# Optimization experiments

Hardware: AMD Instinct MI355X
Metric: run time of the kernel (lower is better)

Reference implementation:

```python
import jax, jax.numpy as jnp
import numpy as np

N_TOTAL = 100000   # total nodes across types
NP_TYPE = 50000    # nodes per type
NP_G = 50000       # nodes per metapath graph
E_G = 500000       # edges per metapath graph
NH = 4             # attention heads
HD = 64            # per-head hidden dim
HID = 64           # shared hidden dim (== in_dim)
D = NH * HD        # 256, semantic attention dim
OUT = 64
T = 20000          # target nodes per metapath


def setup_inputs() -> dict:
    key = jax.random.key(0)
    ks = jax.random.split(key, 20)
    inp = {
        "features0": jax.random.normal(ks[0], (NP_TYPE, 256), jnp.float32),
        "features1": jax.random.normal(ks[1], (NP_TYPE, 256), jnp.float32),
        "fc_W": jax.random.normal(ks[2], (2, HID, 256), jnp.float32) * 0.06,
        "fc_b": jnp.zeros((2, HID), jnp.float32),
        "gat_W": jax.random.normal(ks[3], (2, 2, HID, D), jnp.float32) * 0.12,
        "attn_l": jax.random.normal(ks[4], (2, 2, NH, HD), jnp.float32) * 0.12,
        "attn_r": jax.random.normal(ks[5], (2, 2, NH, HD), jnp.float32) * 0.12,
        "sem_W": jax.random.normal(ks[6], (2, D, D), jnp.float32) * 0.06,
        "sem_b": jnp.zeros((2, D), jnp.float32),
        "sem_q": jax.random.normal(ks[7], (2, D), jnp.float32) * 0.06,
        "fcout_W": jax.random.normal(ks[8], (2, D, OUT), jnp.float32) * 0.06,
        "fcout_b": jnp.zeros((2, OUT), jnp.float32),
        # static index structure (== np.where(type_mask == i))
        "type_idx": jnp.arange(2 * NP_TYPE, dtype=jnp.int32).reshape(2, NP_TYPE),
        "node_idx": jax.random.randint(ks[9], (2, 2, NP_G), 0, N_TOTAL, jnp.int32),
        "edge_src": jax.random.randint(ks[10], (2, 2, E_G), 0, NP_G, jnp.int32),
        "edge_dst": jax.random.randint(ks[11], (2, 2, E_G), 0, NP_G, jnp.int32),
        "tgt_idx": jax.random.randint(ks[12], (2, 2, T), 0, NP_G, jnp.int32),
    }
    return inp


def _gat(h, W, al, ar, src, dst):
    # h: [NP_G, HID] -> multi-head GAT -> [NP_G, NH*HD]
    z = (h @ W).reshape(NP_G, NH, HD)
    el = jnp.sum(z * al, axis=-1)                     # [NP_G, NH]
    er = jnp.sum(z * ar, axis=-1)
    e = jax.nn.leaky_relu(el[src] + er[dst], 0.2)     # [E, NH]
    emax = jax.ops.segment_max(e, dst, num_segments=NP_G)
    emax = jnp.where(jnp.isfinite(emax), emax, 0.0)
    ex = jnp.exp(e - emax[dst])
    denom = jax.ops.segment_sum(ex, dst, num_segments=NP_G)
    alpha = ex / (denom[dst] + 1e-9)                  # edge softmax over in-edges
    out = jax.ops.segment_sum(alpha[:, :, None] * z[src], dst, num_segments=NP_G)
    return jax.nn.elu(out).reshape(NP_G, D)


def _semantic(zs, Wm, bm, qm):
    # zs: [T, M, D] metapath-specific embeddings
    w = jnp.mean(jnp.tanh(zs @ Wm + bm) @ qm, axis=0)  # [M]
    beta = jax.nn.softmax(w)
    return jnp.einsum('tmd,m->td', zs, beta)


def reference(features0, features1, fc_W, fc_b, gat_W, attn_l, attn_r,
              sem_W, sem_b, sem_q, fcout_W, fcout_b,
              type_idx, node_idx, edge_src, edge_dst, tgt_idx):
    # type-based linear + scatter into shared node-feature tensor
    transformed = jnp.zeros((N_TOTAL, HID), dtype=features0.dtype)
    transformed = transformed.at[type_idx[0]].set(features0 @ fc_W[0].T + fc_b[0])
    transformed = transformed.at[type_idx[1]].set(features1 @ fc_W[1].T + fc_b[1])

    outs = []
    for b in range(2):          # two HAN branches (gene, dis)
        metas = []
        for m in range(2):      # metapaths per branch
            h = transformed[node_idx[b, m]]            # gather metapath node feats
            o = _gat(h, gat_W[b, m], attn_l[b, m], attn_r[b, m],
                     edge_src[b, m], edge_dst[b, m])
            metas.append(o[tgt_idx[b, m]])             # select target nodes
        zs = jnp.stack(metas, axis=1)                  # [T, M, D]
        s = _semantic(zs, sem_W[b], sem_b[b], sem_q[b])
        outs.append(s @ fcout_W[b] + fcout_b[b])
    return jnp.stack(outs)  # [2, T, OUT]
```

## Files before the change

### kernel.cpp

```cpp
#include <hip/hip_runtime.h>
#include <math.h>

#define NT     100000
#define NPT    50000
#define NPG    50000
#define EG     500000
#define DD     256
#define TT     20000
#define NPB    196

typedef __attribute__((ext_vector_type(8))) short short8;
typedef __attribute__((ext_vector_type(4))) float f32x4;
typedef unsigned short u16;

#define MFMA16(a, b, c) __builtin_amdgcn_mfma_f32_16x16x32_bf16((a), (b), (c), 0, 0, 0)

__device__ inline unsigned pk2(float x, float y) {
    unsigned a = __float_as_uint(x); a = (a + 0x7FFFu + ((a >> 16) & 1u)) >> 16;
    unsigned b = __float_as_uint(y); b = (b + 0x7FFFu + ((b >> 16) & 1u)) >> 16;
    return (a & 0xFFFFu) | (b << 16);
}
__device__ inline u16 pkb(float x) {
    unsigned a = __float_as_uint(x);
    return (u16)((a + 0x7FFFu + ((a >> 16) & 1u)) >> 16);
}
__device__ inline short8 cvt8(float4 a, float4 b) {
    union { int4 i; short8 s; } u;
    u.i = make_int4((int)pk2(a.x, a.y), (int)pk2(a.z, a.w),
                    (int)pk2(b.x, b.y), (int)pk2(b.z, b.w));
    return u.s;
}
__device__ inline float4 up4(unsigned lo, unsigned hi) {
    float4 r;
    r.x = __uint_as_float(lo << 16);
    r.y = __uint_as_float(lo & 0xFFFF0000u);
    r.z = __uint_as_float(hi << 16);
    r.w = __uint_as_float(hi & 0xFFFF0000u);
    return r;
}
__device__ inline float uplo(unsigned w) { return __uint_as_float(w << 16); }
__device__ inline float uphi(unsigned w) { return __uint_as_float(w & 0xFFFF0000u); }
__device__ inline float ftanh(float x) {
    float e = __expf(2.f * x);
    return 1.f - 2.f * __builtin_amdgcn_rcpf(e + 1.f);
}

__global__ __launch_bounds__(256) void prep_kernel(
    const float* __restrict__ fcW, const float* __restrict__ gatW,
    const float* __restrict__ semW, const float* __restrict__ foW,
    u16* __restrict__ fcWb, u16* __restrict__ gatWb,
    u16* __restrict__ semWb, u16* __restrict__ foWb)
{
    int i = blockIdx.x * 256 + threadIdx.x;
    if (i < 32768) fcWb[i] = pkb(fcW[i]);
    if (i < 65536) {
        int g = i >> 14, rem = i & 16383, n = rem >> 6, k = rem & 63;
        gatWb[i] = pkb(gatW[g * 16384 + k * 256 + n]);
    }
    if (i < 131072) {
        int b = i >> 16, rem = i & 65535, n = rem >> 8, k = rem & 255;
        semWb[i] = pkb(semW[b * 65536 + k * 256 + n]);
    }
    if (i < 32768) {
        int b = i >> 14, rem = i & 16383, n = rem >> 8, k = rem & 255;
        foWb[i] = pkb(foW[b * 16384 + k * 64 + n]);
    }
}

__global__ __launch_bounds__(256) void fc_kernel(
    const float* __restrict__ f0, const float* __restrict__ f1,
    const u16* __restrict__ fcWb, const float* __restrict__ fcb,
    const int* __restrict__ type_idx, u16* __restrict__ tbf)
{
    __shared__ short As[64 * 256];
    __shared__ short Bs[64 * 256];
    int ty = blockIdx.y;
    const float* feat = ty ? f1 : f0;
    const u16* W = fcWb + ty * 64 * 256;
    int tid = threadIdx.x, wv = tid >> 6, l = tid & 63, q = l >> 4, c = l & 15;
    int rbase = blockIdx.x * 64;
    short8 bv[8];
#pragma unroll
    for (int j = 0; j < 8; ++j)
        bv[j] = *(const short8*)&W[(tid + 256 * j) * 8];
    const float* Abase = feat + (size_t)rbase * 256;
#pragma unroll
    for (int half = 0; half < 2; ++half) {
        float4 va[8];
#pragma unroll
        for (int j = 0; j < 8; ++j) {
            int fi = tid + 256 * (half * 8 + j);
            bool okA = (rbase + (fi >> 6)) < NPT;
            va[j] = okA ? *(const float4*)(Abase + (size_t)fi * 4)
                        : (float4){0.f, 0.f, 0.f, 0.f};
        }
#pragma unroll
        for (int j = 0; j < 8; ++j) {
            int fi = tid + 256 * (half * 8 + j);
            int r = fi >> 6, cs = (fi & 63) * 4;
            int2 v = make_int2((int)pk2(va[j].x, va[j].y),
                               (int)pk2(va[j].z, va[j].w));
            *(int2*)&As[r * 256 + (cs ^ ((r & 15) << 3))] = v;
        }
    }
#pragma unroll
    for (int j = 0; j < 8; ++j) {
        int e = tid + 256 * j, r = e >> 5, cs = (e & 31) * 8;
        *(short8*)&Bs[r * 256 + (cs ^ ((r & 15) << 3))] = bv[j];
    }
    __syncthreads();
    short8 af[8];
    int arow = wv * 16 + c;
#pragma unroll
    for (int s = 0; s < 8; ++s)
        af[s] = *(const short8*)&As[arow * 256 + ((q * 8 + 32 * s) ^ (c << 3))];
    f32x4 acc[4];
#pragma unroll
    for (int i = 0; i < 4; ++i) acc[i] = (f32x4){0.f, 0.f, 0.f, 0.f};
#pragma unroll
    for (int s = 0; s < 8; ++s)
#pragma unroll
        for (int t4 = 0; t4 < 4; ++t4)
            acc[t4] = MFMA16(af[s],
                *(const short8*)&Bs[(t4 * 16 + c) * 256 +
                                    ((q * 8 + 32 * s) ^ (c << 3))], acc[t4]);
    int grl = rbase + wv * 16 + q * 4;
#pragma unroll
    for (int t4 = 0; t4 < 4; ++t4) {
        int col = t4 * 16 + c;
        float bvv = fcb[ty * 64 + col];
#pragma unroll
        for (int reg = 0; reg < 4; ++reg) {
            int gr = grl + reg;
            if (gr < NPT) {
                int dest = type_idx[ty * NPT + gr];
                tbf[(size_t)dest * 64 + col] = pkb(acc[t4][reg] + bvv);
            }
        }
    }
}

__global__ __launch_bounds__(256) void z_kernel(
    const u16* __restrict__ tbf, const int* __restrict__ nidx4,
    const u16* __restrict__ gatWb4, const float* __restrict__ al4,
    const float* __restrict__ ar4, u16* __restrict__ zb4,
    float* __restrict__ el4, float* __restrict__ er4, int g0)
{
    __shared__ short Bs[256 * 72];
    int gy = blockIdx.y, g = g0 + gy;
    const int* nidx = nidx4 + (size_t)g * NPG;
    const u16* gatWb = gatWb4 + (size_t)g * 16384;
    const float* al = al4 + g * 256;
    const float* ar = ar4 + g * 256;
    u16* zb = zb4 + (size_t)gy * NPG * 256;
    float* el = el4 + (size_t)gy * NPG * 4;
    float* er = er4 + (size_t)gy * NPG * 4;
    int tid = threadIdx.x, wv = tid >> 6, l = tid & 63, q = l >> 4, c = l & 15;
    short8 bv[8];
#pragma unroll
    for (int j = 0; j < 8; ++j)
        bv[j] = *(const short8*)&gatWb[(tid + 256 * j) * 8];
    int rbase = blockIdx.x * 64;
    int row = rbase + wv * 16 + c;
    bool ok = row < NPG;
    short8 af0 = (short8)(short)0, af1 = (short8)(short)0;
    if (ok) {
        int n = nidx[row];
        const u16* Ap = tbf + (size_t)n * 64 + q * 8;
        af0 = *(const short8*)(Ap);
        af1 = *(const short8*)(Ap + 32);
    }
#pragma unroll
    for (int j = 0; j < 8; ++j) {
        int e = tid + 256 * j, r = e >> 3, kc = (e & 7) * 8;
        *(short8*)&Bs[r * 72 + kc] = bv[j];
    }
    __syncthreads();
    f32x4 acc[16];
    const f32x4 zero = (f32x4){0.f, 0.f, 0.f, 0.f};
#pragma unroll
    for (int t16 = 0; t16 < 16; ++t16) {
        const short* Bp = &Bs[(t16 * 16 + c) * 72 + q * 8];
        acc[t16] = MFMA16(af0, *(const short8*)&Bp[0], zero);
        acc[t16] = MFMA16(af1, *(const short8*)&Bp[32], acc[t16]);
    }
    int grl = rbase + wv * 16 + q * 4;
#pragma unroll
    for (int t16 = 0; t16 < 16; ++t16)
#pragma unroll
        for (int reg = 0; reg < 4; ++reg) {
            int gr = grl + reg;
            if (gr < NPG)
                zb[(size_t)gr * 256 + t16 * 16 + c] = pkb(acc[t16][reg]);
        }
    float pl[4][4], pr[4][4];
#pragma unroll
    for (int reg = 0; reg < 4; ++reg)
#pragma unroll
        for (int h = 0; h < 4; ++h) { pl[reg][h] = 0.f; pr[reg][h] = 0.f; }
#pragma unroll
    for (int t16 = 0; t16 < 16; ++t16) {
        int col = t16 * 16 + c, h = t16 >> 2;
        float alv = al[col], arv = ar[col];
#pragma unroll
        for (int reg = 0; reg < 4; ++reg) {
            pl[reg][h] += acc[t16][reg] * alv;
            pr[reg][h] += acc[t16][reg] * arv;
        }
    }
#pragma unroll
    for (int o = 1; o < 16; o <<= 1)
#pragma unroll
        for (int reg = 0; reg < 4; ++reg)
#pragma unroll
            for (int h = 0; h < 4; ++h) {
                pl[reg][h] += __shfl_xor(pl[reg][h], o);
                pr[reg][h] += __shfl_xor(pr[reg][h], o);
            }
    if (c == 0) {
#pragma unroll
        for (int reg = 0; reg < 4; ++reg) {
            int gr = grl + reg;
            if (gr < NPG) {
                float4 vl = {pl[reg][0], pl[reg][1], pl[reg][2], pl[reg][3]};
                float4 vr = {pr[reg][0], pr[reg][1], pr[reg][2], pr[reg][3]};
                *(float4*)&el[gr * 4] = vl;
                *(float4*)&er[gr * 4] = vr;
            }
        }
    }
}

__global__ __launch_bounds__(256) void mark_kernel(
    const int* __restrict__ tgt, int* __restrict__ tflag4)
{
    int g = blockIdx.y;
    int i = blockIdx.x * 256 + threadIdx.x;
    if (i < TT) tflag4[g * NPG + tgt[(size_t)g * TT + i]] = 1;
}

__global__ __launch_bounds__(256) void count4_kernel(
    const int* __restrict__ dst, const int* __restrict__ tflag4,
    int* __restrict__ deg4)
{
    int g = blockIdx.y;
    int e = blockIdx.x * 256 + threadIdx.x;
    if (e < EG) {
        int d = dst[(size_t)g * EG + e];
        if (tflag4[g * NPG + d]) atomicAdd(&deg4[g * NPG + d], 1);
    }
}

__device__ inline int block_excl_scan(int v, int tid) {
    __shared__ int wtot[4];
    int lane = tid & 63, w = tid >> 6;
    int x = v;
#pragma unroll
    for (int o = 1; o < 64; o <<= 1) {
        int y = __shfl_up(x, o);
        if (lane >= o) x += y;
    }
    if (lane == 63) wtot[w] = x;
    __syncthreads();
    if (tid == 0) {
        int s = 0;
#pragma unroll
        for (int i = 0; i < 4; ++i) { int t = wtot[i]; wtot[i] = s; s += t; }
    }
    __syncthreads();
    return wtot[w] + x - v;
}

__global__ __launch_bounds__(256) void partial4_kernel(
    const int* __restrict__ deg4, int* __restrict__ part4)
{
    int g = blockIdx.y;
    int i = blockIdx.x * 256 + threadIdx.x;
    int v = (i < NPG) ? deg4[g * NPG + i] : 0;
#pragma unroll
    for (int o = 32; o > 0; o >>= 1) v += __shfl_xor(v, o);
    __shared__ int ws4[4];
    if ((threadIdx.x & 63) == 0) ws4[threadIdx.x >> 6] = v;
    __syncthreads();
    if (threadIdx.x == 0)
        part4[g * NPB + blockIdx.x] = ws4[0] + ws4[1] + ws4[2] + ws4[3];
}

__global__ __launch_bounds__(256) void scanp_kernel(
    const int* __restrict__ part4, int* __restrict__ pref4,
    int* __restrict__ offsets4)
{
    int g = blockIdx.y;
    int t = threadIdx.x;
    int v = (t < NPB) ? part4[g * NPB + t] : 0;
    int e = block_excl_scan(v, t);
    if (t < NPB) pref4[g * NPB + t] = e;
    if (t == 255) offsets4[(size_t)g * (NPG + 1) + NPG] = e + v;
}

__global__ __launch_bounds__(256) void distribute_kernel(
    const int* __restrict__ deg4, const int* __restrict__ pref4,
    int* __restrict__ offsets4, int* __restrict__ cursor4)
{
    int g = blockIdx.y;
    int i = blockIdx.x * 256 + threadIdx.x;
    int v = (i < NPG) ? deg4[g * NPG + i] : 0;
    int e = block_excl_scan(v, threadIdx.x);
    if (i < NPG) {
        int off = pref4[g * NPB + blockIdx.x] + e;
        offsets4[(size_t)g * (NPG + 1) + i] = off;
        cursor4[g * NPG + i] = off;
    }
}

__global__ __launch_bounds__(256) void scatter4_kernel(
    const int* __restrict__ dst, const int* __restrict__ src,
    const int* __restrict__ tflag4, int* __restrict__ cursor4,
    int* __restrict__ perm4)
{
    int g = blockIdx.y;
    int e = blockIdx.x * 256 + threadIdx.x;
    if (e < EG) {
        int d = dst[(size_t)g * EG + e];
        if (tflag4[g * NPG + d]) {
            int pos = atomicAdd(&cursor4[g * NPG + d], 1);
            perm4[(size_t)g * EG + pos] = src[(size_t)g * EG + e];
        }
    }
}

__global__ __launch_bounds__(256) void escore_kernel(
    const int* __restrict__ perm4, const int* __restrict__ offsets4,
    const float* __restrict__ el4, float* __restrict__ elp4, int g0)
{
    int gy = blockIdx.y, g = g0 + gy;
    int i = blockIdx.x * 256 + threadIdx.x;
    int total = offsets4[(size_t)g * (NPG + 1) + NPG];
    if (i < total) {
        int s = perm4[(size_t)g * EG + i];
        const float4 v = *(const float4*)&el4[(size_t)gy * NPG * 4 + s * 4];
        *(float4*)&elp4[(size_t)gy * EG * 4 + (size_t)i * 4] = v;
    }
}

__global__ __launch_bounds__(256) void agg_kernel(
    const int* __restrict__ tgt4, const int* __restrict__ offsets4,
    const int* __restrict__ perm4, const float* __restrict__ elp4,
    const float* __restrict__ el4, const float* __restrict__ er4,
    const u16* __restrict__ zb4, u16* __restrict__ metab4, int g0)
{
    int gy = blockIdx.y, g = g0 + gy;
    const int* tgt = tgt4 + (size_t)g * TT;
    const int* offsets = offsets4 + (size_t)g * (NPG + 1);
    const int* perm = perm4 + (size_t)g * EG;
    const float* el = el4 + (size_t)gy * NPG * 4;
    const float* er = er4 + (size_t)gy * NPG * 4;
    const float* elp = elp4 ? elp4 + (size_t)gy * EG * 4 : (const float*)0;
    const u16* zb = zb4 + (size_t)gy * NPG * 256;
    u16* metab = metab4 + (size_t)g * TT * 256;
    int wv = threadIdx.x >> 6, lane = threadIdx.x & 63;
    int t = blockIdx.x * 4 + wv;
    int dstn = tgt[t];
    int start = offsets[dstn];
    int deg = offsets[dstn + 1] - start;
    int pv = perm[start + (lane < deg ? lane : 0)];
    int h1 = lane & 3, e0 = lane >> 2;
    float erv1 = er[dstn * 4 + h1];
    float mx = -INFINITY;
    int h2 = lane >> 4;
    float erv2 = er[dstn * 4 + h2];
    const u16* zrow = zb + (size_t)lane * 4;
    float a0 = 0.f, a1 = 0.f, a2 = 0.f, a3 = 0.f, denom = 0.f;

    if (elp) {
        for (int ee = e0; ee < deg; ee += 16) {
            float v = elp[(start + ee) * 4 + h1] + erv1;
            v = fmaxf(v, 0.2f * v);
            mx = fmaxf(mx, v);
        }
#pragma unroll
        for (int o = 4; o < 64; o <<= 1) mx = fmaxf(mx, __shfl_xor(mx, o));
        float mxh = __shfl(mx, h2);
        int it = 0;
        for (; it + 2 <= deg; it += 2) {
            int s0 = (it < 64) ? __shfl(pv, it) : perm[start + it];
            int s1 = (it + 1 < 64) ? __shfl(pv, it + 1) : perm[start + it + 1];
            float sv0 = elp[(start + it) * 4 + h2];
            float sv1 = elp[(start + it + 1) * 4 + h2];
            uint2 w0 = *(const uint2*)&zrow[(size_t)s0 * 256];
            uint2 w1 = *(const uint2*)&zrow[(size_t)s1 * 256];
            float v0 = sv0 + erv2; v0 = fmaxf(v0, 0.2f * v0);
            float v1 = sv1 + erv2; v1 = fmaxf(v1, 0.2f * v1);
            float ex0 = __expf(v0 - mxh), ex1 = __expf(v1 - mxh);
            denom += ex0 + ex1;
            a0 += ex0 * uplo(w0.x) + ex1 * uplo(w1.x);
            a1 += ex0 * uphi(w0.x) + ex1 * uphi(w1.x);
            a2 += ex0 * uplo(w0.y) + ex1 * uplo(w1.y);
            a3 += ex0 * uphi(w0.y) + ex1 * uphi(w1.y);
        }
        if (it < deg) {
            int s0 = (it < 64) ? __shfl(pv, it) : perm[start + it];
            float v0 = elp[(start + it) * 4 + h2] + erv2;
            v0 = fmaxf(v0, 0.2f * v0);
            float ex0 = __expf(v0 - mxh);
            denom += ex0;
            uint2 w0 = *(const uint2*)&zrow[(size_t)s0 * 256];
            a0 += ex0 * uplo(w0.x); a1 += ex0 * uphi(w0.x);
            a2 += ex0 * uplo(w0.y); a3 += ex0 * uphi(w0.y);
        }
    } else {
        for (int ee = e0; ee < deg; ee += 16) {
            int s = (ee < 64) ? __shfl(pv, ee) : perm[start + ee];
            float v = el[s * 4 + h1] + erv1;
            v = fmaxf(v, 0.2f * v);
            mx = fmaxf(mx, v);
        }
#pragma unroll
        for (int o = 4; o < 64; o <<= 1) mx = fmaxf(mx, __shfl_xor(mx, o));
        float mxh = __shfl(mx, h2);
        for (int it = 0; it < deg; ++it) {
            int s = (it < 64) ? __shfl(pv, it) : perm[start + it];
            float v = el[s * 4 + h2] + erv2;
            v = fmaxf(v, 0.2f * v);
            float ex = __expf(v - mxh);
            denom += ex;
            uint2 w = *(const uint2*)&zrow[(size_t)s * 256];
            a0 += ex * uplo(w.x); a1 += ex * uphi(w.x);
            a2 += ex * uplo(w.y); a3 += ex * uphi(w.y);
        }
    }
    float inv = __builtin_amdgcn_rcpf(denom + 1e-9f);
    float v0 = a0 * inv, v1 = a1 * inv, v2 = a2 * inv, v3 = a3 * inv;
    v0 = v0 > 0.f ? v0 : (__expf(v0) - 1.f);
    v1 = v1 > 0.f ? v1 : (__expf(v1) - 1.f);
    v2 = v2 > 0.f ? v2 : (__expf(v2) - 1.f);
    v3 = v3 > 0.f ? v3 : (__expf(v3) - 1.f);
    uint2 mw;
    mw.x = pk2(v0, v1); mw.y = pk2(v2, v3);
    *(uint2*)&metab[(size_t)t * 256 + lane * 4] = mw;
}

__global__ __launch_bounds__(256) void sem_kernel(
    const u16* __restrict__ metab4, const u16* __restrict__ semWb,
    const float* __restrict__ semb, const float* __restrict__ semq,
    float* __restrict__ wsum4)
{
    __shared__ short Bs[64 * 264];
    __shared__ float bsum;
    int g = blockIdx.y, b = g >> 1;
    const u16* A = metab4 + (size_t)g * TT * 256;
    int tid = threadIdx.x, wv = tid >> 6, l = tid & 63, q = l >> 4, c = l & 15;
    if (tid == 0) bsum = 0.f;
    int rbase = blockIdx.x * 64;
    int row = rbase + wv * 16 + c;
    bool ok = row < TT;
    short8 af[8];
    const u16* Ap = A + (size_t)row * 256 + q * 8;
#pragma unroll
    for (int s = 0; s < 8; ++s)
        af[s] = ok ? *(const short8*)(Ap + 32 * s) : (short8)(short)0;
    float part = 0.f;
    int grl = rbase + wv * 16 + q * 4;
    for (int nq = 0; nq < 4; ++nq) {
        const u16* W = semWb + b * 65536 + nq * 16384;
        short8 bv[8];
#pragma unroll
        for (int j = 0; j < 8; ++j)
            bv[j] = *(const short8*)&W[(tid + 256 * j) * 8];
        __syncthreads();
#pragma unroll
        for (int j = 0; j < 8; ++j) {
            int e = tid + 256 * j, r = e >> 5, kc = (e & 31) * 8;
            *(short8*)&Bs[r * 264 + kc] = bv[j];
        }
        __syncthreads();
        f32x4 acc[4];
#pragma unroll
        for (int i = 0; i < 4; ++i) acc[i] = (f32x4){0.f, 0.f, 0.f, 0.f};
#pragma unroll
        for (int s = 0; s < 8; ++s)
#pragma unroll
            for (int t4 = 0; t4 < 4; ++t4)
                acc[t4] = MFMA16(af[s],
                    *(const short8*)&Bs[(t4 * 16 + c) * 264 + q * 8 + 32 * s], acc[t4]);
#pragma unroll
        for (int t4 = 0; t4 < 4; ++t4) {
            int col = nq * 64 + t4 * 16 + c;
            float bb = semb[b * 256 + col], qq = semq[b * 256 + col];
#pragma unroll
            for (int reg = 0; reg < 4; ++reg)
                if (grl + reg < TT) part += ftanh(acc[t4][reg] + bb) * qq;
        }
    }
    for (int o = 32; o > 0; o >>= 1) part += __shfl_xor(part, o);
    if (l == 0) atomicAdd(&bsum, part);
    __syncthreads();
    if (tid == 0) atomicAdd(&wsum4[g], bsum);
}

__global__ __launch_bounds__(256) void out_kernel(
    const u16* __restrict__ metab4, const float* __restrict__ wsum4,
    const u16* __restrict__ foWb, const float* __restrict__ fob,
    float* __restrict__ out)
{
    __shared__ short Bs[64 * 264];
    int b = blockIdx.y;
    int tid = threadIdx.x, wv = tid >> 6, l = tid & 63, q = l >> 4, c = l & 15;
    float w0 = wsum4[b * 2] * (1.f / TT), w1 = wsum4[b * 2 + 1] * (1.f / TT);
    float mxv = fmaxf(w0, w1);
    float e0 = __expf(w0 - mxv), e1 = __expf(w1 - mxv);
    float inv = 1.f / (e0 + e1);
    float b0 = e0 * inv, b1 = e1 * inv;
    const u16* W = foWb + b * 16384;
    short8 bv[8];
#pragma unroll
    for (int j = 0; j < 8; ++j)
        bv[j] = *(const short8*)&W[(tid + 256 * j) * 8];
    int rbase = blockIdx.x * 64;
    int row = rbase + wv * 16 + c;
    bool ok = row < TT;
    const u16* Ap0 = metab4 + (size_t)(b * 2) * TT * 256 + (size_t)row * 256 + q * 8;
    const u16* Ap1 = Ap0 + (size_t)TT * 256;
    short8 af[8];
#pragma unroll
    for (int half = 0; half < 2; ++half) {
        union { short8 s8; uint4 u; } ua[4], uc[4];
#pragma unroll
        for (int s = 0; s < 4; ++s) {
            int ss = half * 4 + s;
            ua[s].s8 = ok ? *(const short8*)(Ap0 + 32 * ss) : (short8)(short)0;
            uc[s].s8 = ok ? *(const short8*)(Ap1 + 32 * ss) : (short8)(short)0;
        }
        if (half == 0) {
#pragma unroll
            for (int j = 0; j < 8; ++j) {
                int e = tid + 256 * j, r = e >> 5, kc = (e & 31) * 8;
                *(short8*)&Bs[r * 264 + kc] = bv[j];
            }
        }
#pragma unroll
        for (int s = 0; s < 4; ++s) {
            float4 a0 = up4(ua[s].u.x, ua[s].u.y), a1 = up4(ua[s].u.z, ua[s].u.w);
            float4 c0 = up4(uc[s].u.x, uc[s].u.y), c1 = up4(uc[s].u.z, uc[s].u.w);
            float4 v0, v1;
            v0.x = b0 * a0.x + b1 * c0.x; v0.y = b0 * a0.y + b1 * c0.y;
            v0.z = b0 * a0.z + b1 * c0.z; v0.w = b0 * a0.w + b1 * c0.w;
            v1.x = b0 * a1.x + b1 * c1.x; v1.y = b0 * a1.y + b1 * c1.y;
            v1.z = b0 * a1.z + b1 * c1.z; v1.w = b0 * a1.w + b1 * c1.w;
            af[half * 4 + s] = cvt8(v0, v1);
        }
    }
    __syncthreads();
    f32x4 acc[4];
#pragma unroll
    for (int i = 0; i < 4; ++i) acc[i] = (f32x4){0.f, 0.f, 0.f, 0.f};
#pragma unroll
    for (int s = 0; s < 8; ++s)
#pragma unroll
        for (int t4 = 0; t4 < 4; ++t4)
            acc[t4] = MFMA16(af[s],
                *(const short8*)&Bs[(t4 * 16 + c) * 264 + q * 8 + 32 * s], acc[t4]);
    int grl = rbase + wv * 16 + q * 4;
#pragma unroll
    for (int t4 = 0; t4 < 4; ++t4) {
        int col = t4 * 16 + c;
        float bvv = fob[b * 64 + col];
#pragma unroll
        for (int reg = 0; reg < 4; ++reg) {
            int gr = grl + reg;
            if (gr < TT)
                out[(size_t)b * TT * 64 + (size_t)gr * 64 + col] = acc[t4][reg] + bvv;
        }
    }
}

extern "C" void kernel_launch(void* const* d_in, const int* in_sizes, int n_in,
                              void* d_out, int out_size, void* d_ws, size_t ws_size,
                              hipStream_t stream)
{
    const float* f0    = (const float*)d_in[0];
    const float* f1    = (const float*)d_in[1];
    const float* fcW   = (const float*)d_in[2];
    const float* fcb   = (const float*)d_in[3];
    const float* gatW  = (const float*)d_in[4];
    const float* al    = (const float*)d_in[5];
    const float* ar    = (const float*)d_in[6];
    const float* semW  = (const float*)d_in[7];
    const float* semb  = (const float*)d_in[8];
    const float* semq  = (const float*)d_in[9];
    const float* foW   = (const float*)d_in[10];
    const float* fob   = (const float*)d_in[11];
    const int* type_idx = (const int*)d_in[12];
    const int* node_idx = (const int*)d_in[13];
    const int* edge_src = (const int*)d_in[14];
    const int* edge_dst = (const int*)d_in[15];
    const int* tgt_idx  = (const int*)d_in[16];
    float* out = (float*)d_out;

    char* ws = (char*)d_ws;
    size_t off = 0;
    auto alloc = [&](size_t bytes) -> void* {
        void* p = ws + off;
        off = (off + bytes + 255) & ~(size_t)255;
        return p;
    };
    u16*   tbf         = (u16*)alloc((size_t)NT * 64 * 2);
    u16*   metab4      = (u16*)alloc((size_t)4 * TT * 256 * 2);
    float* wsum4       = (float*)alloc(64);
    u16*   fcWb        = (u16*)alloc(32768 * 2);
    u16*   gatWb       = (u16*)alloc(65536 * 2);
    u16*   semWb       = (u16*)alloc(131072 * 2);
    u16*   foWb        = (u16*)alloc(32768 * 2);
    int*   deg4        = (int*)alloc((size_t)4 * NPG * 4);
    int*   tflag4      = (int*)alloc((size_t)4 * NPG * 4);
    int*   offsets4    = (int*)alloc((size_t)4 * (NPG + 1) * 4);
    int*   cursor4     = (int*)alloc((size_t)4 * NPG * 4);
    int*   perm4       = (int*)alloc((size_t)4 * EG * 4);
    int*   part4       = (int*)alloc((size_t)4 * NPB * 4);
    int*   pref4       = (int*)alloc((size_t)4 * NPB * 4);
    const size_t perg_base = (size_t)NPG * 256 * 2 + 2 * (size_t)NPG * 4 * 4 + 768;
    const size_t perg_elp  = perg_base + (size_t)EG * 16 + 256;
    int GPB = 1; bool use_elp = false;
    {
        size_t rem = (ws_size > off) ? ws_size - off : 0;
        if      (rem >= 4 * perg_elp)  { GPB = 4; use_elp = true;  }
        else if (rem >= 4 * perg_base) { GPB = 4; use_elp = false; }
        else if (rem >= 2 * perg_elp)  { GPB = 2; use_elp = true;  }
        else if (rem >= 2 * perg_base) { GPB = 2; use_elp = false; }
        else if (rem >= 1 * perg_elp)  { GPB = 1; use_elp = true;  }
    }
    u16*   zb          = (u16*)alloc((size_t)GPB * NPG * 256 * 2);
    float* el          = (float*)alloc((size_t)GPB * NPG * 4 * 4);
    float* er          = (float*)alloc((size_t)GPB * NPG * 4 * 4);
    float* elp         = use_elp ? (float*)alloc((size_t)GPB * EG * 16) : (float*)0;

    const int eblocks = (EG + 255) / 256;
    const int tblocks = (TT + 255) / 256;

    prep_kernel<<<512, 256, 0, stream>>>(fcW, gatW, semW, foW,
                                         fcWb, gatWb, semWb, foWb);

    hipMemsetAsync(deg4, 0, (size_t)4 * NPG * 4, stream);
    hipMemsetAsync(tflag4, 0, (size_t)4 * NPG * 4, stream);
    hipMemsetAsync(wsum4, 0, 16, stream);
    mark_kernel<<<dim3(tblocks, 4), 256, 0, stream>>>(tgt_idx, tflag4);
    count4_kernel<<<dim3(eblocks, 4), 256, 0, stream>>>(edge_dst, tflag4, deg4);
    partial4_kernel<<<dim3(NPB, 4), 256, 0, stream>>>(deg4, part4);
    scanp_kernel<<<dim3(1, 4), 256, 0, stream>>>(part4, pref4, offsets4);
    distribute_kernel<<<dim3(NPB, 4), 256, 0, stream>>>(deg4, pref4, offsets4,
                                                        cursor4);
    scatter4_kernel<<<dim3(eblocks, 4), 256, 0, stream>>>(edge_dst, edge_src,
                                                          tflag4, cursor4, perm4);

    fc_kernel<<<dim3(782, 2), 256, 0, stream>>>(f0, f1, fcWb, fcb, type_idx, tbf);
    for (int g0 = 0; g0 < 4; g0 += GPB) {
        z_kernel<<<dim3(782, GPB), 256, 0, stream>>>(
            tbf, node_idx, gatWb, al, ar, zb, el, er, g0);
        if (elp)
            escore_kernel<<<dim3(eblocks, GPB), 256, 0, stream>>>(
                perm4, offsets4, el, elp, g0);
        agg_kernel<<<dim3(TT / 4, GPB), 256, 0, stream>>>(
            tgt_idx, offsets4, perm4, elp, el, er, zb, metab4, g0);
    }
    sem_kernel<<<dim3(313, 4), 256, 0, stream>>>(metab4, semWb, semb, semq,
                                                 wsum4);
    out_kernel<<<dim3(313, 2), 256, 0, stream>>>(metab4, wsum4, foWb, fob, out);
}
```

Measured before the change: 445.0 us.

## Precompute leaky-relu edge scores and process two targets per wavefront in aggregation

The scatter pass now also records each edge's destination, so the edge-score kernel can add er[dst] and apply leaky ReLU once per edge. The aggregation kernel then reads finished scores instead of recomputing them. The aggregation kernel also handles two target nodes per wavefront with interleaved loops, which doubles the independent gathers in flight to hide memory latency. The cost is an extra edge-sized index buffer, an extra gather of er in the score kernel, more registers, and idle work when the two targets' degrees differ.

```diff
diff --git a/kernel.cpp b/kernel.cpp
--- a/kernel.cpp
+++ b/kernel.cpp
@@ -316,7 +316,7 @@
 __global__ __launch_bounds__(256) void scatter4_kernel(
     const int* __restrict__ dst, const int* __restrict__ src,
     const int* __restrict__ tflag4, int* __restrict__ cursor4,
-    int* __restrict__ perm4)
+    int* __restrict__ perm4, int* __restrict__ dpm4)
 {
     int g = blockIdx.y;
     int e = blockIdx.x * 256 + threadIdx.x;
@@ -325,20 +325,29 @@
         if (tflag4[g * NPG + d]) {
             int pos = atomicAdd(&cursor4[g * NPG + d], 1);
             perm4[(size_t)g * EG + pos] = src[(size_t)g * EG + e];
+            dpm4[(size_t)g * EG + pos] = d;
         }
     }
 }
 
 __global__ __launch_bounds__(256) void escore_kernel(
-    const int* __restrict__ perm4, const int* __restrict__ offsets4,
-    const float* __restrict__ el4, float* __restrict__ elp4, int g0)
+    const int* __restrict__ perm4, const int* __restrict__ dpm4,
+    const int* __restrict__ offsets4, const float* __restrict__ el4,
+    const float* __restrict__ er4, float* __restrict__ elp4, int g0)
 {
     int gy = blockIdx.y, g = g0 + gy;
     int i = blockIdx.x * 256 + threadIdx.x;
     int total = offsets4[(size_t)g * (NPG + 1) + NPG];
     if (i < total) {
         int s = perm4[(size_t)g * EG + i];
-        const float4 v = *(const float4*)&el4[(size_t)gy * NPG * 4 + s * 4];
+        int d = dpm4[(size_t)g * EG + i];
+        float4 a = *(const float4*)&el4[(size_t)gy * NPG * 4 + s * 4];
+        float4 b = *(const float4*)&er4[(size_t)gy * NPG * 4 + d * 4];
+        float4 v;
+        v.x = a.x + b.x; v.x = fmaxf(v.x, 0.2f * v.x);
+        v.y = a.y + b.y; v.y = fmaxf(v.y, 0.2f * v.y);
+        v.z = a.z + b.z; v.z = fmaxf(v.z, 0.2f * v.z);
+        v.w = a.w + b.w; v.w = fmaxf(v.w, 0.2f * v.w);
         *(float4*)&elp4[(size_t)gy * EG * 4 + (size_t)i * 4] = v;
     }
 }
@@ -359,85 +368,133 @@
     const u16* zb = zb4 + (size_t)gy * NPG * 256;
     u16* metab = metab4 + (size_t)g * TT * 256;
     int wv = threadIdx.x >> 6, lane = threadIdx.x & 63;
-    int t = blockIdx.x * 4 + wv;
-    int dstn = tgt[t];
-    int start = offsets[dstn];
-    int deg = offsets[dstn + 1] - start;
-    int pv = perm[start + (lane < deg ? lane : 0)];
-    int h1 = lane & 3, e0 = lane >> 2;
-    float erv1 = er[dstn * 4 + h1];
-    float mx = -INFINITY;
-    int h2 = lane >> 4;
-    float erv2 = er[dstn * 4 + h2];
+    int t0 = blockIdx.x * 8 + wv * 2, t1 = t0 + 1;
+    int d0 = tgt[t0], d1 = tgt[t1];
+    int st0 = offsets[d0], de0 = offsets[d0 + 1] - st0;
+    int st1 = offsets[d1], de1 = offsets[d1 + 1] - st1;
+    int pv0 = perm[st0 + (lane < de0 ? lane : 0)];
+    int pv1 = perm[st1 + (lane < de1 ? lane : 0)];
+    int h1 = lane & 3, e0l = lane >> 2, h2 = lane >> 4;
     const u16* zrow = zb + (size_t)lane * 4;
-    float a0 = 0.f, a1 = 0.f, a2 = 0.f, a3 = 0.f, denom = 0.f;
+    float mx0 = -INFINITY, mx1 = -INFINITY;
+    float a00 = 0.f, a01 = 0.f, a02 = 0.f, a03 = 0.f, dn0 = 0.f;
+    float a10 = 0.f, a11 = 0.f, a12 = 0.f, a13 = 0.f, dn1 = 0.f;
 
     if (elp) {
-        for (int ee = e0; ee < deg; ee += 16) {
-            float v = elp[(start + ee) * 4 + h1] + erv1;
-            v = fmaxf(v, 0.2f * v);
-            mx = fmaxf(mx, v);
-        }
-#pragma unroll
-        for (int o = 4; o < 64; o <<= 1) mx = fmaxf(mx, __shfl_xor(mx, o));
-        float mxh = __shfl(mx, h2);
+        for (int ee = e0l; ee < de0; ee += 16)
+            mx0 = fmaxf(mx0, elp[(st0 + ee) * 4 + h1]);
+        for (int ee = e0l; ee < de1; ee += 16)
+            mx1 = fmaxf(mx1, elp[(st1 + ee) * 4 + h1]);
+#pragma unroll
+        for (int o = 4; o < 64; o <<= 1) {
+            mx0 = fmaxf(mx0, __shfl_xor(mx0, o));
+            mx1 = fmaxf(mx1, __shfl_xor(mx1, o));
+        }
+        float mxh0 = __shfl(mx0, h2), mxh1 = __shfl(mx1, h2);
+        int degmax = de0 > de1 ? de0 : de1;
         int it = 0;
-        for (; it + 2 <= deg; it += 2) {
-            int s0 = (it < 64) ? __shfl(pv, it) : perm[start + it];
-            int s1 = (it + 1 < 64) ? __shfl(pv, it + 1) : perm[start + it + 1];
-            float sv0 = elp[(start + it) * 4 + h2];
-            float sv1 = elp[(start + it + 1) * 4 + h2];
+        for (; it + 2 <= degmax; it += 2) {
+            int i1 = it + 1;
+            bool b00 = it < de0, b01 = i1 < de0;
+            bool b10 = it < de1, b11 = i1 < de1;
+            int s00 = b00 ? ((it < 64) ? __shfl(pv0, it) : perm[st0 + it]) : 0;
+            int s01 = b01 ? ((i1 < 64) ? __shfl(pv0, i1) : perm[st0 + i1]) : 0;
+            int s10 = b10 ? ((it < 64) ? __shfl(pv1, it) : perm[st1 + it]) : 0;
+            int s11 = b11 ? ((i1 < 64) ? __shfl(pv1, i1) : perm[st1 + i1]) : 0;
+            float v00 = b00 ? elp[(st0 + it) * 4 + h2] : 0.f;
+            float v01 = b01 ? elp[(st0 + i1) * 4 + h2] : 0.f;
+            float v10 = b10 ? elp[(st1 + it) * 4 + h2] : 0.f;
+            float v11 = b11 ? elp[(st1 + i1) * 4 + h2] : 0.f;
+            uint2 w00 = *(const uint2*)&zrow[(size_t)s00 * 256];
+            uint2 w01 = *(const uint2*)&zrow[(size_t)s01 * 256];
+            uint2 w10 = *(const uint2*)&zrow[(size_t)s10 * 256];
+            uint2 w11 = *(const uint2*)&zrow[(size_t)s11 * 256];
+            float ex00 = b00 ? __expf(v00 - mxh0) : 0.f;
+            float ex01 = b01 ? __expf(v01 - mxh0) : 0.f;
+            float ex10 = b10 ? __expf(v10 - mxh1) : 0.f;
+            float ex11 = b11 ? __expf(v11 - mxh1) : 0.f;
+            dn0 += ex00 + ex01; dn1 += ex10 + ex11;
+            a00 += ex00 * uplo(w00.x) + ex01 * uplo(w01.x);
+            a01 += ex00 * uphi(w00.x) + ex01 * uphi(w01.x);
+            a02 += ex00 * uplo(w00.y) + ex01 * uplo(w01.y);
+            a03 += ex00 * uphi(w00.y) + ex01 * uphi(w01.y);
+            a10 += ex10 * uplo(w10.x) + ex11 * uplo(w11.x);
+            a11 += ex10 * uphi(w10.x) + ex11 * uphi(w11.x);
+            a12 += ex10 * uplo(w10.y) + ex11 * uplo(w11.y);
+            a13 += ex10 * uphi(w10.y) + ex11 * uphi(w11.y);
+        }
+        if (it < degmax) {
+            bool b0 = it < de0, b1 = it < de1;
+            int s0 = b0 ? ((it < 64) ? __shfl(pv0, it) : perm[st0 + it]) : 0;
+            int s1 = b1 ? ((it < 64) ? __shfl(pv1, it) : perm[st1 + it]) : 0;
+            float v0 = b0 ? elp[(st0 + it) * 4 + h2] : 0.f;
+            float v1 = b1 ? elp[(st1 + it) * 4 + h2] : 0.f;
             uint2 w0 = *(const uint2*)&zrow[(size_t)s0 * 256];
             uint2 w1 = *(const uint2*)&zrow[(size_t)s1 * 256];
-            float v0 = sv0 + erv2; v0 = fmaxf(v0, 0.2f * v0);
-            float v1 = sv1 + erv2; v1 = fmaxf(v1, 0.2f * v1);
-            float ex0 = __expf(v0 - mxh), ex1 = __expf(v1 - mxh);
-            denom += ex0 + ex1;
-            a0 += ex0 * uplo(w0.x) + ex1 * uplo(w1.x);
-            a1 += ex0 * uphi(w0.x) + ex1 * uphi(w1.x);
-            a2 += ex0 * uplo(w0.y) + ex1 * uplo(w1.y);
-            a3 += ex0 * uphi(w0.y) + ex1 * uphi(w1.y);
-        }
-        if (it < deg) {
-            int s0 = (it < 64) ? __shfl(pv, it) : perm[start + it];
-            float v0 = elp[(start + it) * 4 + h2] + erv2;
-            v0 = fmaxf(v0, 0.2f * v0);
-            float ex0 = __expf(v0 - mxh);
-            denom += ex0;
-            uint2 w0 = *(const uint2*)&zrow[(size_t)s0 * 256];
-            a0 += ex0 * uplo(w0.x); a1 += ex0 * uphi(w0.x);
-            a2 += ex0 * uplo(w0.y); a3 += ex0 * uphi(w0.y);
+            float ex0 = b0 ? __expf(v0 - mxh0) : 0.f;
+            float ex1 = b1 ? __expf(v1 - mxh1) : 0.f;
+            dn0 += ex0; dn1 += ex1;
+            a00 += ex0 * uplo(w0.x); a01 += ex0 * uphi(w0.x);
+            a02 += ex0 * uplo(w0.y); a03 += ex0 * uphi(w0.y);
+            a10 += ex1 * uplo(w1.x); a11 += ex1 * uphi(w1.x);
+            a12 += ex1 * uplo(w1.y); a13 += ex1 * uphi(w1.y);
         }
     } else {
-        for (int ee = e0; ee < deg; ee += 16) {
-            int s = (ee < 64) ? __shfl(pv, ee) : perm[start + ee];
-            float v = el[s * 4 + h1] + erv1;
-            v = fmaxf(v, 0.2f * v);
-            mx = fmaxf(mx, v);
-        }
-#pragma unroll
-        for (int o = 4; o < 64; o <<= 1) mx = fmaxf(mx, __shfl_xor(mx, o));
-        float mxh = __shfl(mx, h2);
-        for (int it = 0; it < deg; ++it) {
-            int s = (it < 64) ? __shfl(pv, it) : perm[start + it];
-            float v = el[s * 4 + h2] + erv2;
-            v = fmaxf(v, 0.2f * v);
-            float ex = __expf(v - mxh);
-            denom += ex;
+        float er0 = er[d0 * 4 + h1], er1 = er[d1 * 4 + h1];
+        for (int ee = e0l; ee < de0; ee += 16) {
+            int s = (ee < 64) ? __shfl(pv0, ee) : perm[st0 + ee];
+            float v = el[s * 4 + h1] + er0; v = fmaxf(v, 0.2f * v);
+            mx0 = fmaxf(mx0, v);
+        }
+        for (int ee = e0l; ee < de1; ee += 16) {
+            int s = (ee < 64) ? __shfl(pv1, ee) : perm[st1 + ee];
+            float v = el[s * 4 + h1] + er1; v = fmaxf(v, 0.2f * v);
+            mx1 = fmaxf(mx1, v);
+        }
+#pragma unroll
+        for (int o = 4; o < 64; o <<= 1) {
+            mx0 = fmaxf(mx0, __shfl_xor(mx0, o));
+            mx1 = fmaxf(mx1, __shfl_xor(mx1, o));
+        }
+        float mxh0 = __shfl(mx0, h2), mxh1 = __shfl(mx1, h2);
+        float erv20 = er[d0 * 4 + h2], erv21 = er[d1 * 4 + h2];
+        for (int it = 0; it < de0; ++it) {
+            int s = (it < 64) ? __shfl(pv0, it) : perm[st0 + it];
+            float v = el[s * 4 + h2] + erv20; v = fmaxf(v, 0.2f * v);
+            float ex = __expf(v - mxh0);
+            dn0 += ex;
             uint2 w = *(const uint2*)&zrow[(size_t)s * 256];
-            a0 += ex * uplo(w.x); a1 += ex * uphi(w.x);
-            a2 += ex * uplo(w.y); a3 += ex * uphi(w.y);
-        }
-    }
-    float inv = __builtin_amdgcn_rcpf(denom + 1e-9f);
-    float v0 = a0 * inv, v1 = a1 * inv, v2 = a2 * inv, v3 = a3 * inv;
+            a00 += ex * uplo(w.x); a01 += ex * uphi(w.x);
+            a02 += ex * uplo(w.y); a03 += ex * uphi(w.y);
+        }
+        for (int it = 0; it < de1; ++it) {
+            int s = (it < 64) ? __shfl(pv1, it) : perm[st1 + it];
+            float v = el[s * 4 + h2] + erv21; v = fmaxf(v, 0.2f * v);
+            float ex = __expf(v - mxh1);
+            dn1 += ex;
+            uint2 w = *(const uint2*)&zrow[(size_t)s * 256];
+            a10 += ex * uplo(w.x); a11 += ex * uphi(w.x);
+            a12 += ex * uplo(w.y); a13 += ex * uphi(w.y);
+        }
+    }
+    float inv0 = __builtin_amdgcn_rcpf(dn0 + 1e-9f);
+    float inv1 = __builtin_amdgcn_rcpf(dn1 + 1e-9f);
+    float v0 = a00 * inv0, v1 = a01 * inv0, v2 = a02 * inv0, v3 = a03 * inv0;
     v0 = v0 > 0.f ? v0 : (__expf(v0) - 1.f);
     v1 = v1 > 0.f ? v1 : (__expf(v1) - 1.f);
     v2 = v2 > 0.f ? v2 : (__expf(v2) - 1.f);
     v3 = v3 > 0.f ? v3 : (__expf(v3) - 1.f);
     uint2 mw;
     mw.x = pk2(v0, v1); mw.y = pk2(v2, v3);
-    *(uint2*)&metab[(size_t)t * 256 + lane * 4] = mw;
+    *(uint2*)&metab[(size_t)t0 * 256 + lane * 4] = mw;
+    float u0 = a10 * inv1, u1 = a11 * inv1, u2 = a12 * inv1, u3 = a13 * inv1;
+    u0 = u0 > 0.f ? u0 : (__expf(u0) - 1.f);
+    u1 = u1 > 0.f ? u1 : (__expf(u1) - 1.f);
+    u2 = u2 > 0.f ? u2 : (__expf(u2) - 1.f);
+    u3 = u3 > 0.f ? u3 : (__expf(u3) - 1.f);
+    uint2 mw1;
+    mw1.x = pk2(u0, u1); mw1.y = pk2(u2, u3);
+    *(uint2*)&metab[(size_t)t1 * 256 + lane * 4] = mw1;
 }
 
 __global__ __launch_bounds__(256) void sem_kernel(
@@ -616,6 +673,7 @@
     int*   offsets4    = (int*)alloc((size_t)4 * (NPG + 1) * 4);
     int*   cursor4     = (int*)alloc((size_t)4 * NPG * 4);
     int*   perm4       = (int*)alloc((size_t)4 * EG * 4);
+    int*   dpm4        = (int*)alloc((size_t)4 * EG * 4);
     int*   part4       = (int*)alloc((size_t)4 * NPB * 4);
     int*   pref4       = (int*)alloc((size_t)4 * NPB * 4);
     const size_t perg_base = (size_t)NPG * 256 * 2 + 2 * (size_t)NPG * 4 * 4 + 768;
@@ -650,7 +708,8 @@
     distribute_kernel<<<dim3(NPB, 4), 256, 0, stream>>>(deg4, pref4, offsets4,
                                                         cursor4);
     scatter4_kernel<<<dim3(eblocks, 4), 256, 0, stream>>>(edge_dst, edge_src,
-                                                          tflag4, cursor4, perm4);
+                                                          tflag4, cursor4,
+                                                          perm4, dpm4);
 
     fc_kernel<<<dim3(782, 2), 256, 0, stream>>>(f0, f1, fcWb, fcb, type_idx, tbf);
     for (int g0 = 0; g0 < 4; g0 += GPB) {
@@ -658,8 +717,8 @@
             tbf, node_idx, gatWb, al, ar, zb, el, er, g0);
         if (elp)
             escore_kernel<<<dim3(eblocks, GPB), 256, 0, stream>>>(
-                perm4, offsets4, el, elp, g0);
-        agg_kernel<<<dim3(TT / 4, GPB), 256, 0, stream>>>(
+                perm4, dpm4, offsets4, el, er, elp, g0);
+        agg_kernel<<<dim3(TT / 8, GPB), 256, 0, stream>>>(
             tgt_idx, offsets4, perm4, elp, el, er, zb, metab4, g0);
     }
     sem_kernel<<<dim3(313, 4), 256, 0, stream>>>(metab4, semWb, semb, semq,
```

Result: slower. 468.9 us (+5.4%).

## Precompute full edge scores in escore, pack target offsets, persistent-wave agg loop

Applied to the files above, without the earlier changes.

The scatter pass now also records each edge's destination, so escore_kernel can compute the full leaky-relu score (el[src]+er[dst]) per sorted edge and agg no longer adds er or applies leaky-relu. A new tpack kernel stores each target's (start,end) offsets as an int2, which removes the dependent tgt→offsets lookup in agg. agg_kernel becomes a grid-stride persistent loop over targets with a fixed block count, and its inner loop is unrolled by 4 to keep more independent gathers in flight. In exchange it adds an extra EG-sized int array, an extra write in scatter, one more small launch, and possible load imbalance from the fixed grid.

```diff
diff --git a/kernel.cpp b/kernel.cpp
--- a/kernel.cpp
+++ b/kernel.cpp
@@ -8,6 +8,7 @@
 #define DD     256
 #define TT     20000
 #define NPB    196
+#define AGGB   2048
 
 typedef __attribute__((ext_vector_type(8))) short short8;
 typedef __attribute__((ext_vector_type(4))) float f32x4;
@@ -316,7 +317,7 @@
 __global__ __launch_bounds__(256) void scatter4_kernel(
     const int* __restrict__ dst, const int* __restrict__ src,
     const int* __restrict__ tflag4, int* __restrict__ cursor4,
-    int* __restrict__ perm4)
+    int* __restrict__ perm4, int* __restrict__ dpm4)
 {
     int g = blockIdx.y;
     int e = blockIdx.x * 256 + threadIdx.x;
@@ -325,119 +326,146 @@
         if (tflag4[g * NPG + d]) {
             int pos = atomicAdd(&cursor4[g * NPG + d], 1);
             perm4[(size_t)g * EG + pos] = src[(size_t)g * EG + e];
-        }
+            dpm4[(size_t)g * EG + pos] = d;
+        }
+    }
+}
+
+__global__ __launch_bounds__(256) void tpack_kernel(
+    const int* __restrict__ tgt4, const int* __restrict__ offsets4,
+    int2* __restrict__ tp4)
+{
+    int g = blockIdx.y;
+    int i = blockIdx.x * 256 + threadIdx.x;
+    if (i < TT) {
+        int d = tgt4[(size_t)g * TT + i];
+        const int* o = offsets4 + (size_t)g * (NPG + 1) + d;
+        tp4[(size_t)g * TT + i] = make_int2(o[0], o[1]);
     }
 }
 
 __global__ __launch_bounds__(256) void escore_kernel(
-    const int* __restrict__ perm4, const int* __restrict__ offsets4,
-    const float* __restrict__ el4, float* __restrict__ elp4, int g0)
+    const int* __restrict__ perm4, const int* __restrict__ dpm4,
+    const int* __restrict__ offsets4, const float* __restrict__ el4,
+    const float* __restrict__ er4, float* __restrict__ elp4, int g0)
 {
     int gy = blockIdx.y, g = g0 + gy;
     int i = blockIdx.x * 256 + threadIdx.x;
     int total = offsets4[(size_t)g * (NPG + 1) + NPG];
     if (i < total) {
         int s = perm4[(size_t)g * EG + i];
-        const float4 v = *(const float4*)&el4[(size_t)gy * NPG * 4 + s * 4];
+        int d = dpm4[(size_t)g * EG + i];
+        float4 a = *(const float4*)&el4[(size_t)gy * NPG * 4 + s * 4];
+        float4 b = *(const float4*)&er4[(size_t)gy * NPG * 4 + d * 4];
+        float4 v;
+        v.x = a.x + b.x; v.x = fmaxf(v.x, 0.2f * v.x);
+        v.y = a.y + b.y; v.y = fmaxf(v.y, 0.2f * v.y);
+        v.z = a.z + b.z; v.z = fmaxf(v.z, 0.2f * v.z);
+        v.w = a.w + b.w; v.w = fmaxf(v.w, 0.2f * v.w);
         *(float4*)&elp4[(size_t)gy * EG * 4 + (size_t)i * 4] = v;
     }
 }
 
 __global__ __launch_bounds__(256) void agg_kernel(
-    const int* __restrict__ tgt4, const int* __restrict__ offsets4,
+    const int* __restrict__ tgt4, const int2* __restrict__ tp4,
     const int* __restrict__ perm4, const float* __restrict__ elp4,
     const float* __restrict__ el4, const float* __restrict__ er4,
     const u16* __restrict__ zb4, u16* __restrict__ metab4, int g0)
 {
     int gy = blockIdx.y, g = g0 + gy;
-    const int* tgt = tgt4 + (size_t)g * TT;
-    const int* offsets = offsets4 + (size_t)g * (NPG + 1);
+    const int2* tp = tp4 + (size_t)g * TT;
     const int* perm = perm4 + (size_t)g * EG;
-    const float* el = el4 + (size_t)gy * NPG * 4;
-    const float* er = er4 + (size_t)gy * NPG * 4;
     const float* elp = elp4 ? elp4 + (size_t)gy * EG * 4 : (const float*)0;
     const u16* zb = zb4 + (size_t)gy * NPG * 256;
     u16* metab = metab4 + (size_t)g * TT * 256;
-    int wv = threadIdx.x >> 6, lane = threadIdx.x & 63;
-    int t = blockIdx.x * 4 + wv;
-    int dstn = tgt[t];
-    int start = offsets[dstn];
-    int deg = offsets[dstn + 1] - start;
-    int pv = perm[start + (lane < deg ? lane : 0)];
-    int h1 = lane & 3, e0 = lane >> 2;
-    float erv1 = er[dstn * 4 + h1];
-    float mx = -INFINITY;
-    int h2 = lane >> 4;
-    float erv2 = er[dstn * 4 + h2];
+    int lane = threadIdx.x & 63;
+    int h1 = lane & 3, e0l = lane >> 2, h2 = lane >> 4;
     const u16* zrow = zb + (size_t)lane * 4;
-    float a0 = 0.f, a1 = 0.f, a2 = 0.f, a3 = 0.f, denom = 0.f;
-
-    if (elp) {
-        for (int ee = e0; ee < deg; ee += 16) {
-            float v = elp[(start + ee) * 4 + h1] + erv1;
-            v = fmaxf(v, 0.2f * v);
-            mx = fmaxf(mx, v);
-        }
-#pragma unroll
-        for (int o = 4; o < 64; o <<= 1) mx = fmaxf(mx, __shfl_xor(mx, o));
-        float mxh = __shfl(mx, h2);
-        int it = 0;
-        for (; it + 2 <= deg; it += 2) {
-            int s0 = (it < 64) ? __shfl(pv, it) : perm[start + it];
-            int s1 = (it + 1 < 64) ? __shfl(pv, it + 1) : perm[start + it + 1];
-            float sv0 = elp[(start + it) * 4 + h2];
-            float sv1 = elp[(start + it + 1) * 4 + h2];
-            uint2 w0 = *(const uint2*)&zrow[(size_t)s0 * 256];
-            uint2 w1 = *(const uint2*)&zrow[(size_t)s1 * 256];
-            float v0 = sv0 + erv2; v0 = fmaxf(v0, 0.2f * v0);
-            float v1 = sv1 + erv2; v1 = fmaxf(v1, 0.2f * v1);
-            float ex0 = __expf(v0 - mxh), ex1 = __expf(v1 - mxh);
-            denom += ex0 + ex1;
-            a0 += ex0 * uplo(w0.x) + ex1 * uplo(w1.x);
-            a1 += ex0 * uphi(w0.x) + ex1 * uphi(w1.x);
-            a2 += ex0 * uplo(w0.y) + ex1 * uplo(w1.y);
-            a3 += ex0 * uphi(w0.y) + ex1 * uphi(w1.y);
-        }
-        if (it < deg) {
-            int s0 = (it < 64) ? __shfl(pv, it) : perm[start + it];
-            float v0 = elp[(start + it) * 4 + h2] + erv2;
-            v0 = fmaxf(v0, 0.2f * v0);
-            float ex0 = __expf(v0 - mxh);
-            denom += ex0;
-            uint2 w0 = *(const uint2*)&zrow[(size_t)s0 * 256];
-            a0 += ex0 * uplo(w0.x); a1 += ex0 * uphi(w0.x);
-            a2 += ex0 * uplo(w0.y); a3 += ex0 * uphi(w0.y);
-        }
-    } else {
-        for (int ee = e0; ee < deg; ee += 16) {
-            int s = (ee < 64) ? __shfl(pv, ee) : perm[start + ee];
-            float v = el[s * 4 + h1] + erv1;
-            v = fmaxf(v, 0.2f * v);
-            mx = fmaxf(mx, v);
-        }
-#pragma unroll
-        for (int o = 4; o < 64; o <<= 1) mx = fmaxf(mx, __shfl_xor(mx, o));
-        float mxh = __shfl(mx, h2);
-        for (int it = 0; it < deg; ++it) {
-            int s = (it < 64) ? __shfl(pv, it) : perm[start + it];
-            float v = el[s * 4 + h2] + erv2;
-            v = fmaxf(v, 0.2f * v);
-            float ex = __expf(v - mxh);
-            denom += ex;
-            uint2 w = *(const uint2*)&zrow[(size_t)s * 256];
-            a0 += ex * uplo(w.x); a1 += ex * uphi(w.x);
-            a2 += ex * uplo(w.y); a3 += ex * uphi(w.y);
-        }
-    }
-    float inv = __builtin_amdgcn_rcpf(denom + 1e-9f);
-    float v0 = a0 * inv, v1 = a1 * inv, v2 = a2 * inv, v3 = a3 * inv;
-    v0 = v0 > 0.f ? v0 : (__expf(v0) - 1.f);
-    v1 = v1 > 0.f ? v1 : (__expf(v1) - 1.f);
-    v2 = v2 > 0.f ? v2 : (__expf(v2) - 1.f);
-    v3 = v3 > 0.f ? v3 : (__expf(v3) - 1.f);
-    uint2 mw;
-    mw.x = pk2(v0, v1); mw.y = pk2(v2, v3);
-    *(uint2*)&metab[(size_t)t * 256 + lane * 4] = mw;
+    const int nwaves = AGGB * 4;
+    int wid0 = blockIdx.x * 4 + (threadIdx.x >> 6);
+
+    for (int t = wid0; t < TT; t += nwaves) {
+        int2 se = tp[t];
+        int start = se.x, deg = se.y - se.x;
+        int pv = perm[start + (lane < deg ? lane : 0)];
+        float mx = -INFINITY;
+        float a0 = 0.f, a1 = 0.f, a2 = 0.f, a3 = 0.f, dn = 0.f;
+        if (elp) {
+            const float* es = elp + (size_t)start * 4;
+            for (int ee = e0l; ee < deg; ee += 16)
+                mx = fmaxf(mx, es[ee * 4 + h1]);
+#pragma unroll
+            for (int o = 4; o < 64; o <<= 1) mx = fmaxf(mx, __shfl_xor(mx, o));
+            float mxh = __shfl(mx, h2);
+            int it = 0, dega = deg & ~3;
+            for (; it < dega; it += 4) {
+                int s0 = (it + 0 < 64) ? __shfl(pv, it + 0) : perm[start + it + 0];
+                int s1 = (it + 1 < 64) ? __shfl(pv, it + 1) : perm[start + it + 1];
+                int s2 = (it + 2 < 64) ? __shfl(pv, it + 2) : perm[start + it + 2];
+                int s3 = (it + 3 < 64) ? __shfl(pv, it + 3) : perm[start + it + 3];
+                float c0 = es[(it + 0) * 4 + h2];
+                float c1 = es[(it + 1) * 4 + h2];
+                float c2 = es[(it + 2) * 4 + h2];
+                float c3 = es[(it + 3) * 4 + h2];
+                uint2 w0 = *(const uint2*)&zrow[(size_t)s0 * 256];
+                uint2 w1 = *(const uint2*)&zrow[(size_t)s1 * 256];
+                uint2 w2 = *(const uint2*)&zrow[(size_t)s2 * 256];
+                uint2 w3 = *(const uint2*)&zrow[(size_t)s3 * 256];
+                float x0 = __expf(c0 - mxh), x1 = __expf(c1 - mxh);
+                float x2 = __expf(c2 - mxh), x3 = __expf(c3 - mxh);
+                dn += (x0 + x1) + (x2 + x3);
+                a0 += x0 * uplo(w0.x) + x1 * uplo(w1.x)
+                    + x2 * uplo(w2.x) + x3 * uplo(w3.x);
+                a1 += x0 * uphi(w0.x) + x1 * uphi(w1.x)
+                    + x2 * uphi(w2.x) + x3 * uphi(w3.x);
+                a2 += x0 * uplo(w0.y) + x1 * uplo(w1.y)
+                    + x2 * uplo(w2.y) + x3 * uplo(w3.y);
+                a3 += x0 * uphi(w0.y) + x1 * uphi(w1.y)
+                    + x2 * uphi(w2.y) + x3 * uphi(w3.y);
+            }
+            for (; it < deg; ++it) {
+                int s = (it < 64) ? __shfl(pv, it) : perm[start + it];
+                float c = es[it * 4 + h2];
+                uint2 w = *(const uint2*)&zrow[(size_t)s * 256];
+                float x = __expf(c - mxh);
+                dn += x;
+                a0 += x * uplo(w.x); a1 += x * uphi(w.x);
+                a2 += x * uplo(w.y); a3 += x * uphi(w.y);
+            }
+        } else {
+            const float* el = el4 + (size_t)gy * NPG * 4;
+            const float* er = er4 + (size_t)gy * NPG * 4;
+            int dstn = tgt4[(size_t)g * TT + t];
+            float erv1 = er[dstn * 4 + h1];
+            for (int ee = e0l; ee < deg; ee += 16) {
+                int s = (ee < 64) ? __shfl(pv, ee) : perm[start + ee];
+                float v = el[s * 4 + h1] + erv1; v = fmaxf(v, 0.2f * v);
+                mx = fmaxf(mx, v);
+            }
+#pragma unroll
+            for (int o = 4; o < 64; o <<= 1) mx = fmaxf(mx, __shfl_xor(mx, o));
+            float mxh = __shfl(mx, h2);
+            float erv2 = er[dstn * 4 + h2];
+            for (int it = 0; it < deg; ++it) {
+                int s = (it < 64) ? __shfl(pv, it) : perm[start + it];
+                float v = el[s * 4 + h2] + erv2; v = fmaxf(v, 0.2f * v);
+                float x = __expf(v - mxh);
+                dn += x;
+                uint2 w = *(const uint2*)&zrow[(size_t)s * 256];
+                a0 += x * uplo(w.x); a1 += x * uphi(w.x);
+                a2 += x * uplo(w.y); a3 += x * uphi(w.y);
+            }
+        }
+        float inv = __builtin_amdgcn_rcpf(dn + 1e-9f);
+        float v0 = a0 * inv, v1 = a1 * inv, v2 = a2 * inv, v3 = a3 * inv;
+        v0 = v0 > 0.f ? v0 : (__expf(v0) - 1.f);
+        v1 = v1 > 0.f ? v1 : (__expf(v1) - 1.f);
+        v2 = v2 > 0.f ? v2 : (__expf(v2) - 1.f);
+        v3 = v3 > 0.f ? v3 : (__expf(v3) - 1.f);
+        uint2 mw;
+        mw.x = pk2(v0, v1); mw.y = pk2(v2, v3);
+        *(uint2*)&metab[(size_t)t * 256 + lane * 4] = mw;
+    }
 }
 
 __global__ __launch_bounds__(256) void sem_kernel(
@@ -616,6 +644,8 @@
     int*   offsets4    = (int*)alloc((size_t)4 * (NPG + 1) * 4);
     int*   cursor4     = (int*)alloc((size_t)4 * NPG * 4);
     int*   perm4       = (int*)alloc((size_t)4 * EG * 4);
+    int*   dpm4        = (int*)alloc((size_t)4 * EG * 4);
+    int2*  tp4         = (int2*)alloc((size_t)4 * TT * 8);
     int*   part4       = (int*)alloc((size_t)4 * NPB * 4);
     int*   pref4       = (int*)alloc((size_t)4 * NPB * 4);
     const size_t perg_base = (size_t)NPG * 256 * 2 + 2 * (size_t)NPG * 4 * 4 + 768;
@@ -649,8 +679,10 @@
     scanp_kernel<<<dim3(1, 4), 256, 0, stream>>>(part4, pref4, offsets4);
     distribute_kernel<<<dim3(NPB, 4), 256, 0, stream>>>(deg4, pref4, offsets4,
                                                         cursor4);
+    tpack_kernel<<<dim3(tblocks, 4), 256, 0, stream>>>(tgt_idx, offsets4, tp4);
     scatter4_kernel<<<dim3(eblocks, 4), 256, 0, stream>>>(edge_dst, edge_src,
-                                                          tflag4, cursor4, perm4);
+                                                          tflag4, cursor4,
+                                                          perm4, dpm4);
 
     fc_kernel<<<dim3(782, 2), 256, 0, stream>>>(f0, f1, fcWb, fcb, type_idx, tbf);
     for (int g0 = 0; g0 < 4; g0 += GPB) {
@@ -658,9 +690,9 @@
             tbf, node_idx, gatWb, al, ar, zb, el, er, g0);
         if (elp)
             escore_kernel<<<dim3(eblocks, GPB), 256, 0, stream>>>(
-                perm4, offsets4, el, elp, g0);
-        agg_kernel<<<dim3(TT / 4, GPB), 256, 0, stream>>>(
-            tgt_idx, offsets4, perm4, elp, el, er, zb, metab4, g0);
+                perm4, dpm4, offsets4, el, er, elp, g0);
+        agg_kernel<<<dim3(AGGB, GPB), 256, 0, stream>>>(
+            tgt_idx, tp4, perm4, elp, el, er, zb, metab4, g0);
     }
     sem_kernel<<<dim3(313, 4), 256, 0, stream>>>(metab4, semWb, semb, semq,
                                                  wsum4);
```

New measurement: 454.2 us. 2.1% more time.
